# Performance work log

Measured on AMD Instinct MI355X. Metric: run time of the kernel, lower is better.

Reference implementation:

```python
import jax, jax.numpy as jnp
import numpy as np

B, T, D_IN, D_OUT = 4, 2048, 1024, 1024

def setup_inputs() -> dict:
    key = jax.random.key(0)
    k0, k1, k2, k3 = jax.random.split(key, 4)
    s = 1.0 / np.sqrt(D_IN)
    return {
        "x": jax.random.normal(k0, (B, T, D_IN), dtype=jnp.float32),
        "w_query": jax.random.normal(k1, (D_OUT, D_IN), dtype=jnp.float32) * s,
        "w_key": jax.random.normal(k2, (D_OUT, D_IN), dtype=jnp.float32) * s,
        "w_value": jax.random.normal(k3, (D_OUT, D_IN), dtype=jnp.float32) * s,
    }

def reference(x, w_query, w_key, w_value):
    # Linear (no bias): y = x @ W.T, W has shape (d_out, d_in)
    q = jnp.einsum('btd,od->bto', x, w_query)   # (B,T,d_out)
    k = jnp.einsum('btd,od->bto', x, w_key)
    v = jnp.einsum('btd,od->bto', x, w_value)
    scale = 1.0 / jnp.sqrt(jnp.asarray(k.shape[-1], dtype=x.dtype))
    scores = jnp.einsum('bqo,bko->bqk', q, k) * scale  # (B,T,T)
    t = scores.shape[-1]
    causal = jnp.tril(jnp.ones((t, t), dtype=bool))    # True = keep
    scores = jnp.where(causal, scores, -jnp.inf)
    weights = jax.nn.softmax(scores, axis=-1)
    # dropout rate is 0.0 -> identity
    context = jnp.einsum('bqk,bko->bqo', weights, v)   # (B,T,d_out)
    return context
```

## Files before the change

### kernel.cpp

```cpp
#include <hip/hip_runtime.h>
#include <hip/hip_bf16.h>

#define NB 4
#define TT 2048
#define DD 1024
#define MM (NB*TT)

using f32x4  = __attribute__((ext_vector_type(4))) float;
using bf16x8 = __attribute__((ext_vector_type(8))) __bf16;
using u16x8  = __attribute__((ext_vector_type(8))) unsigned short;

__device__ __forceinline__ unsigned short f2b(float f) {
  __hip_bfloat16 h = __float2bfloat16(f);
  return *reinterpret_cast<unsigned short*>(&h);
}

__device__ __forceinline__ float b2f(unsigned short u) {
  __hip_bfloat16 h = *reinterpret_cast<__hip_bfloat16*>(&u);
  return __bfloat162float(h);
}

__device__ __forceinline__ void gld_lds16(const void* g, void* l) {
  __builtin_amdgcn_global_load_lds(
      (const __attribute__((address_space(1))) void*)g,
      (__attribute__((address_space(3))) void*)l, 16, 0, 0);
}

__global__ void k_cvt(const float* __restrict__ src, unsigned short* __restrict__ dst, int n4) {
  int i = blockIdx.x * blockDim.x + threadIdx.x;
  int stride = gridDim.x * blockDim.x;
  for (; i < n4; i += stride) {
    float4 v = reinterpret_cast<const float4*>(src)[i];
    ushort4 o;
    o.x = f2b(v.x); o.y = f2b(v.y); o.z = f2b(v.z); o.w = f2b(v.w);
    reinterpret_cast<ushort4*>(dst)[i] = o;
  }
}

__launch_bounds__(256)
__global__ void k_qkv(const unsigned short* __restrict__ xb,
                      const unsigned short* __restrict__ wqb,
                      const unsigned short* __restrict__ wkb,
                      const unsigned short* __restrict__ wvb,
                      unsigned short* __restrict__ Qb,
                      unsigned short* __restrict__ Kb,
                      unsigned short* __restrict__ Vt) {
  __shared__ __align__(16) unsigned short As[128*32];
  __shared__ __align__(16) unsigned short Bs[128*32];
  const int tid = threadIdx.x;
  const int l = tid & 63, wid = tid >> 6;
  const int z = blockIdx.z;
  const unsigned short* W = (z == 0) ? wqb : (z == 1) ? wkb : wvb;
  unsigned short* out = (z == 0) ? Qb : (z == 1) ? Kb : Vt;
  const long m0 = (long)blockIdx.x * 128;
  const long n0 = (long)blockIdx.y * 128;
  const int l15 = l & 15, l4 = l >> 4;
  const int wr = (wid >> 1) * 64, wc = (wid & 1) * 64;

  const int lrow = tid >> 2;
  const int lcol = (tid & 3) * 8;
  const unsigned short* Ap = xb + (m0 + lrow) * DD + lcol;
  const unsigned short* Wp = W  + (n0 + lrow) * DD + lcol;
  unsigned short* AsW = &As[wid * 512];
  unsigned short* BsW = &Bs[wid * 512];

  f32x4 acc[4][4] = {};

  for (int k0 = 0; k0 < DD; k0 += 32) {
    __syncthreads();
    gld_lds16(Ap + k0,           AsW);
    gld_lds16(Ap + 64*DD + k0,   AsW + 2048);
    gld_lds16(Wp + k0,           BsW);
    gld_lds16(Wp + 64*DD + k0,   BsW + 2048);
    __syncthreads();
    bf16x8 af[4], bfr[4];
    #pragma unroll
    for (int mi = 0; mi < 4; ++mi)
      af[mi] = *reinterpret_cast<const bf16x8*>(&As[(wr + mi*16 + l15)*32 + l4*8]);
    #pragma unroll
    for (int ni = 0; ni < 4; ++ni)
      bfr[ni] = *reinterpret_cast<const bf16x8*>(&Bs[(wc + ni*16 + l15)*32 + l4*8]);
    #pragma unroll
    for (int mi = 0; mi < 4; ++mi)
      #pragma unroll
      for (int ni = 0; ni < 4; ++ni)
        acc[mi][ni] = __builtin_amdgcn_mfma_f32_16x16x32_bf16(af[mi], bfr[ni], acc[mi][ni], 0, 0, 0);
  }

  if (z < 2) {
    #pragma unroll
    for (int mi = 0; mi < 4; ++mi)
      #pragma unroll
      for (int ni = 0; ni < 4; ++ni)
        #pragma unroll
        for (int r = 0; r < 4; ++r) {
          long row = m0 + wr + mi*16 + l4*4 + r;
          long col = n0 + wc + ni*16 + l15;
          out[row * DD + col] = f2b(acc[mi][ni][r]);
        }
  } else {
    #pragma unroll
    for (int mi = 0; mi < 4; ++mi)
      #pragma unroll
      for (int ni = 0; ni < 4; ++ni)
        #pragma unroll
        for (int r = 0; r < 4; ++r) {
          long row = m0 + wr + mi*16 + l4*4 + r;
          long col = n0 + wc + ni*16 + l15;
          long b = row >> 11, t = row & (TT - 1);
          out[(b * DD + col) * TT + t] = f2b(acc[mi][ni][r]);
        }
  }
}

__launch_bounds__(256)
__global__ void k_scores(const unsigned short* __restrict__ Qb,
                         const unsigned short* __restrict__ Kb,
                         unsigned short* __restrict__ S) {
  __shared__ __align__(16) unsigned short As[128*32];
  __shared__ __align__(16) unsigned short Bs[128*32];
  const int tid = threadIdx.x;
  const int l = tid & 63, wid = tid >> 6;
  const int l15 = l & 15, l4 = l >> 4;
  const int wr = (wid >> 1) * 64, wc = (wid & 1) * 64;

  const int b = blockIdx.x / 136;
  int t = blockIdx.x % 136;
  int qi = 0;
  while ((qi + 1) * (qi + 2) / 2 <= t) qi++;
  const int ki = t - qi * (qi + 1) / 2;

  const size_t arow0 = (size_t)b * TT + qi * 128;
  const size_t brow0 = (size_t)b * TT + ki * 128;

  const int lrow = tid >> 2;
  const int lcol = (tid & 3) * 8;
  const unsigned short* Ap = Qb + (arow0 + lrow) * DD + lcol;
  const unsigned short* Bp = Kb + (brow0 + lrow) * DD + lcol;
  unsigned short* AsW = &As[wid * 512];
  unsigned short* BsW = &Bs[wid * 512];

  f32x4 acc[4][4] = {};

  for (int k0 = 0; k0 < DD; k0 += 32) {
    __syncthreads();
    gld_lds16(Ap + k0,           AsW);
    gld_lds16(Ap + 64*DD + k0,   AsW + 2048);
    gld_lds16(Bp + k0,           BsW);
    gld_lds16(Bp + 64*DD + k0,   BsW + 2048);
    __syncthreads();
    bf16x8 af[4], bfr[4];
    #pragma unroll
    for (int mi = 0; mi < 4; ++mi)
      af[mi] = *reinterpret_cast<const bf16x8*>(&As[(wr + mi*16 + l15)*32 + l4*8]);
    #pragma unroll
    for (int ni = 0; ni < 4; ++ni)
      bfr[ni] = *reinterpret_cast<const bf16x8*>(&Bs[(wc + ni*16 + l15)*32 + l4*8]);
    #pragma unroll
    for (int mi = 0; mi < 4; ++mi)
      #pragma unroll
      for (int ni = 0; ni < 4; ++ni)
        acc[mi][ni] = __builtin_amdgcn_mfma_f32_16x16x32_bf16(af[mi], bfr[ni], acc[mi][ni], 0, 0, 0);
  }

  const float scale = 0.03125f;
  #pragma unroll
  for (int mi = 0; mi < 4; ++mi)
    #pragma unroll
    for (int ni = 0; ni < 4; ++ni)
      #pragma unroll
      for (int r = 0; r < 4; ++r) {
        int row = wr + mi*16 + l4*4 + r;
        int col = wc + ni*16 + l15;
        int gq = qi*128 + row, gk = ki*128 + col;
        float v = (gk > gq) ? -1e30f : acc[mi][ni][r] * scale;
        S[((size_t)b * TT + gq) * TT + gk] = f2b(v);
      }
}

__launch_bounds__(256)
__global__ void k_softmax(unsigned short* __restrict__ S, float* __restrict__ rl) {
  const int tid = threadIdx.x;
  const int w = tid >> 6, l = tid & 63;
  const int row = blockIdx.x * 4 + w;
  const int b = row >> 11, q = row & (TT - 1);
  unsigned short* Srow = S + ((size_t)b * TT + q) * TT;
  const int width = ((q >> 7) + 1) << 7;

  float v[4][8];
  bool has[4];
  float mx = -1e30f;
  #pragma unroll
  for (int c = 0; c < 4; ++c) {
    const int off = c * 512 + l * 8;
    has[c] = off < width;
    if (has[c]) {
      u16x8 u = *reinterpret_cast<const u16x8*>(&Srow[off]);
      #pragma unroll
      for (int j = 0; j < 8; ++j) { v[c][j] = b2f(u[j]); mx = fmaxf(mx, v[c][j]); }
    }
  }
  #pragma unroll
  for (int mm = 1; mm < 64; mm <<= 1) mx = fmaxf(mx, __shfl_xor(mx, mm));

  float s = 0.f;
  #pragma unroll
  for (int c = 0; c < 4; ++c) {
    if (has[c]) {
      u16x8 u;
      #pragma unroll
      for (int j = 0; j < 8; ++j) {
        float p = __expf(v[c][j] - mx);
        s += p;
        u[j] = f2b(p);
      }
      *reinterpret_cast<u16x8*>(&Srow[c * 512 + l * 8]) = u;
    }
  }
  #pragma unroll
  for (int mm = 1; mm < 64; mm <<= 1) s += __shfl_xor(s, mm);
  if (l == 0) rl[row] = 1.0f / s;
}

__launch_bounds__(256)
__global__ void k_pv(const unsigned short* __restrict__ P,
                     const unsigned short* __restrict__ Vt,
                     const float* __restrict__ rl,
                     float* __restrict__ O) {
  __shared__ __align__(16) unsigned short As[128*32];
  __shared__ __align__(16) unsigned short Bs[128*32];
  const int tid = threadIdx.x;
  const int l = tid & 63, wid = tid >> 6;
  const int l15 = l & 15, l4 = l >> 4;
  const int wr = (wid >> 1) * 64, wc = (wid & 1) * 64;

  const int qi = 15 - (blockIdx.x >> 5);
  const int di = (blockIdx.x >> 2) & 7;
  const int b  = blockIdx.x & 3;
  const int KEXT = (qi + 1) * 128;

  const int lrow = tid >> 2;
  const int lcol = (tid & 3) * 8;
  const unsigned short* Ap = P  + ((size_t)b * TT + qi * 128 + lrow) * TT + lcol;
  const unsigned short* Bp = Vt + ((size_t)b * DD + di * 128 + lrow) * TT + lcol;
  unsigned short* AsW = &As[wid * 512];
  unsigned short* BsW = &Bs[wid * 512];

  f32x4 acc[4][4] = {};

  for (int k0 = 0; k0 < KEXT; k0 += 32) {
    __syncthreads();
    gld_lds16(Ap + k0,           AsW);
    gld_lds16(Ap + 64*TT + k0,   AsW + 2048);
    gld_lds16(Bp + k0,           BsW);
    gld_lds16(Bp + 64*TT + k0,   BsW + 2048);
    __syncthreads();
    bf16x8 af[4], bfr[4];
    #pragma unroll
    for (int mi = 0; mi < 4; ++mi)
      af[mi] = *reinterpret_cast<const bf16x8*>(&As[(wr + mi*16 + l15)*32 + l4*8]);
    #pragma unroll
    for (int ni = 0; ni < 4; ++ni)
      bfr[ni] = *reinterpret_cast<const bf16x8*>(&Bs[(wc + ni*16 + l15)*32 + l4*8]);
    #pragma unroll
    for (int mi = 0; mi < 4; ++mi)
      #pragma unroll
      for (int ni = 0; ni < 4; ++ni)
        acc[mi][ni] = __builtin_amdgcn_mfma_f32_16x16x32_bf16(af[mi], bfr[ni], acc[mi][ni], 0, 0, 0);
  }

  #pragma unroll
  for (int mi = 0; mi < 4; ++mi)
    #pragma unroll
    for (int ni = 0; ni < 4; ++ni)
      #pragma unroll
      for (int r = 0; r < 4; ++r) {
        int row = wr + mi*16 + l4*4 + r;
        int col = wc + ni*16 + l15;
        size_t q = (size_t)qi * 128 + row;
        O[((size_t)b * TT + q) * DD + di * 128 + col] =
            acc[mi][ni][r] * rl[(size_t)b * TT + q];
      }
}

extern "C" void kernel_launch(void* const* d_in, const int* in_sizes, int n_in,
                              void* d_out, int out_size, void* d_ws, size_t ws_size,
                              hipStream_t stream) {
  const float* x  = (const float*)d_in[0];
  const float* wq = (const float*)d_in[1];
  const float* wk = (const float*)d_in[2];
  const float* wv = (const float*)d_in[3];
  unsigned short* ws  = (unsigned short*)d_ws;
  unsigned short* Qb  = ws;
  unsigned short* Kb  = Qb + (size_t)MM * DD;
  unsigned short* Vt  = Kb + (size_t)MM * DD;
  unsigned short* Sb  = Vt + (size_t)MM * DD;
  unsigned short* xb  = Sb;
  unsigned short* wqb = xb + (size_t)MM * DD;
  unsigned short* wkb = wqb + (size_t)DD * DD;
  unsigned short* wvb = wkb + (size_t)DD * DD;
  float* rl = (float*)(Sb + (size_t)NB * TT * TT);
  float* out = (float*)d_out;

  k_cvt<<<1024, 256, 0, stream>>>(x,  xb,  MM*DD/4);
  k_cvt<<<256,  256, 0, stream>>>(wq, wqb, DD*DD/4);
  k_cvt<<<256,  256, 0, stream>>>(wk, wkb, DD*DD/4);
  k_cvt<<<256,  256, 0, stream>>>(wv, wvb, DD*DD/4);
  k_qkv<<<dim3(MM/128, DD/128, 3), 256, 0, stream>>>(xb, wqb, wkb, wvb, Qb, Kb, Vt);
  k_scores<<<544, 256, 0, stream>>>(Qb, Kb, Sb);
  k_softmax<<<MM/4, 256, 0, stream>>>(Sb, rl);
  k_pv<<<512, 256, 0, stream>>>(Sb, Vt, rl, out);
}
```

Before: 187.4 us.

## Rewrite QKV projection as 256x256 double-buffered GEMM and fuse conversion kernels

Merges the four fp32-to-bf16 conversion launches into one kernel. Replaces the 128x128 single-buffered QKV GEMM with a 256x256 tile, 8-wave kernel that uses 128KB of LDS. Global-to-LDS loads are double-buffered with a K tile of 64, and prefetch is interleaved with split MFMA phases through raw barriers, waitcnt and setprio. LDS reads use an XOR swizzle to avoid bank conflicts. The aim is to hide memory latency and raise MFMA utilization, at the cost of complex manual synchronization and a smaller grid of 384 blocks, about one wave on 256 CUs.

```diff
diff --git a/kernel.cpp b/kernel.cpp
--- a/kernel.cpp
+++ b/kernel.cpp
@@ -26,89 +26,187 @@
       (__attribute__((address_space(3))) void*)l, 16, 0, 0);
 }
 
-__global__ void k_cvt(const float* __restrict__ src, unsigned short* __restrict__ dst, int n4) {
+__device__ __forceinline__ void bar() {
+  asm volatile("" ::: "memory");
+  __builtin_amdgcn_s_barrier();
+  asm volatile("" ::: "memory");
+}
+
+__global__ void k_cvt4(const float* __restrict__ x,  const float* __restrict__ wq,
+                       const float* __restrict__ wk, const float* __restrict__ wv,
+                       unsigned short* __restrict__ xb, unsigned short* __restrict__ wqb,
+                       unsigned short* __restrict__ wkb, unsigned short* __restrict__ wvb) {
+  const int nx = MM*DD/4, nw = DD*DD/4;
+  const int ntot = nx + 3*nw;
   int i = blockIdx.x * blockDim.x + threadIdx.x;
   int stride = gridDim.x * blockDim.x;
-  for (; i < n4; i += stride) {
-    float4 v = reinterpret_cast<const float4*>(src)[i];
+  for (; i < ntot; i += stride) {
+    const float* s; unsigned short* d; int j;
+    if (i < nx)            { s = x;  d = xb;  j = i; }
+    else if (i < nx + nw)  { s = wq; d = wqb; j = i - nx; }
+    else if (i < nx + 2*nw){ s = wk; d = wkb; j = i - nx - nw; }
+    else                   { s = wv; d = wvb; j = i - nx - 2*nw; }
+    float4 v = reinterpret_cast<const float4*>(s)[j];
     ushort4 o;
     o.x = f2b(v.x); o.y = f2b(v.y); o.z = f2b(v.z); o.w = f2b(v.w);
-    reinterpret_cast<ushort4*>(dst)[i] = o;
-  }
-}
-
-__launch_bounds__(256)
-__global__ void k_qkv(const unsigned short* __restrict__ xb,
-                      const unsigned short* __restrict__ wqb,
-                      const unsigned short* __restrict__ wkb,
-                      const unsigned short* __restrict__ wvb,
-                      unsigned short* __restrict__ Qb,
-                      unsigned short* __restrict__ Kb,
-                      unsigned short* __restrict__ Vt) {
-  __shared__ __align__(16) unsigned short As[128*32];
-  __shared__ __align__(16) unsigned short Bs[128*32];
+    reinterpret_cast<ushort4*>(d)[j] = o;
+  }
+}
+
+__launch_bounds__(512, 2)
+__global__ void k_qkv8(const unsigned short* __restrict__ xb,
+                       const unsigned short* __restrict__ wqb,
+                       const unsigned short* __restrict__ wkb,
+                       const unsigned short* __restrict__ wvb,
+                       unsigned short* __restrict__ Qb,
+                       unsigned short* __restrict__ Kb,
+                       unsigned short* __restrict__ Vt) {
+  __shared__ __align__(16) char Lds[131072];
   const int tid = threadIdx.x;
   const int l = tid & 63, wid = tid >> 6;
+  const int l15 = l & 15, l4 = l >> 4;
+  const int wm = wid >> 2, wn = wid & 3;
   const int z = blockIdx.z;
   const unsigned short* W = (z == 0) ? wqb : (z == 1) ? wkb : wvb;
-  unsigned short* out = (z == 0) ? Qb : (z == 1) ? Kb : Vt;
-  const long m0 = (long)blockIdx.x * 128;
-  const long n0 = (long)blockIdx.y * 128;
-  const int l15 = l & 15, l4 = l >> 4;
-  const int wr = (wid >> 1) * 64, wc = (wid & 1) * 64;
-
-  const int lrow = tid >> 2;
-  const int lcol = (tid & 3) * 8;
-  const unsigned short* Ap = xb + (m0 + lrow) * DD + lcol;
-  const unsigned short* Wp = W  + (n0 + lrow) * DD + lcol;
-  unsigned short* AsW = &As[wid * 512];
-  unsigned short* BsW = &Bs[wid * 512];
-
-  f32x4 acc[4][4] = {};
-
-  for (int k0 = 0; k0 < DD; k0 += 32) {
-    __syncthreads();
-    gld_lds16(Ap + k0,           AsW);
-    gld_lds16(Ap + 64*DD + k0,   AsW + 2048);
-    gld_lds16(Wp + k0,           BsW);
-    gld_lds16(Wp + 64*DD + k0,   BsW + 2048);
-    __syncthreads();
-    bf16x8 af[4], bfr[4];
-    #pragma unroll
-    for (int mi = 0; mi < 4; ++mi)
-      af[mi] = *reinterpret_cast<const bf16x8*>(&As[(wr + mi*16 + l15)*32 + l4*8]);
-    #pragma unroll
-    for (int ni = 0; ni < 4; ++ni)
-      bfr[ni] = *reinterpret_cast<const bf16x8*>(&Bs[(wc + ni*16 + l15)*32 + l4*8]);
-    #pragma unroll
-    for (int mi = 0; mi < 4; ++mi)
-      #pragma unroll
-      for (int ni = 0; ni < 4; ++ni)
-        acc[mi][ni] = __builtin_amdgcn_mfma_f32_16x16x32_bf16(af[mi], bfr[ni], acc[mi][ni], 0, 0, 0);
-  }
+  const size_t m0 = (size_t)blockIdx.x * 256;
+  const size_t n0 = (size_t)blockIdx.y * 256;
+
+  int srow[2], scb[2];
+  #pragma unroll
+  for (int j = 0; j < 2; ++j) {
+    int d  = (j*512 + tid) * 16;
+    int sd = d ^ (((d >> 9) & 1) << 5);
+    srow[j] = sd >> 7;
+    scb[j]  = sd & 127;
+  }
+  const char* pA[2][2]; const char* pB[2][2];
+  #pragma unroll
+  for (int h = 0; h < 2; ++h)
+    #pragma unroll
+    for (int j = 0; j < 2; ++j) {
+      pA[h][j] = (const char*)xb + ((m0 + h*128 + srow[j]) * DD) * 2 + scb[j];
+      pB[h][j] = (const char*)W  + ((n0 + h*128 + srow[j]) * DD) * 2 + scb[j];
+    }
+  char* ldsA = Lds;
+  char* ldsB = Lds + 65536;
+
+#define STG(p, ldsr, slot, half, kt) do {                                         \
+    gld_lds16(p[half][0] + (size_t)(kt)*128,                                      \
+              (ldsr) + (slot)*32768 + (half)*16384 + wid*1024);                   \
+    gld_lds16(p[half][1] + (size_t)(kt)*128,                                      \
+              (ldsr) + (slot)*32768 + (half)*16384 + 8192 + wid*1024);            \
+  } while (0)
+
+#define KTQ 16
+  STG(pA, ldsA, 0, 0, 0);
+  STG(pA, ldsA, 0, 1, 0);
+  STG(pB, ldsB, 0, 0, 0);
+  STG(pB, ldsB, 0, 1, 0);
+  STG(pA, ldsA, 1, 0, 1);
+  STG(pA, ldsA, 1, 1, 1);
+  STG(pB, ldsB, 1, 0, 1);
+  asm volatile("s_waitcnt vmcnt(6)" ::: "memory");
+  bar();
+
+  f32x4 acc[8][4] = {};
+  bf16x8 af[8][2], bf[2][2];
+
+#define TILE(t, S) do {                                                           \
+    const int tn = ((t)+1 < KTQ) ? (t)+1 : 0;                                     \
+    const int t2 = ((t)+2 < KTQ) ? (t)+2 : 0;                                     \
+           \
+    _Pragma("unroll") for (int m = 0; m < 8; ++m)                                 \
+      _Pragma("unroll") for (int kk = 0; kk < 2; ++kk) {                          \
+        int lg = m*2048 + l15*128 + kk*64 + l4*16;                                \
+        int ph = lg ^ (((lg >> 9) & 1) << 5);                                     \
+        af[m][kk] = *(const bf16x8*)(ldsA + (S)*32768 + wm*16384 + ph); }         \
+    _Pragma("unroll") for (int n = 0; n < 2; ++n)                                 \
+      _Pragma("unroll") for (int kk = 0; kk < 2; ++kk) {                          \
+        int lg = ((wn&1)*64 + n*16 + l15)*128 + kk*64 + l4*16;                    \
+        int ph = lg ^ (((lg >> 9) & 1) << 5);                                     \
+        bf[n][kk] = *(const bf16x8*)(ldsB + (S)*32768 + (wn>>1)*16384 + ph); }    \
+    STG(pB, ldsB, (S)^1, 1, tn);                                                  \
+    bar();                                                                        \
+    asm volatile("s_waitcnt lgkmcnt(0)" ::: "memory");                            \
+    __builtin_amdgcn_sched_barrier(0);                                            \
+    __builtin_amdgcn_s_setprio(1);                                                \
+    _Pragma("unroll") for (int m = 0; m < 4; ++m)                                 \
+      _Pragma("unroll") for (int n = 0; n < 2; ++n)                               \
+        _Pragma("unroll") for (int kk = 0; kk < 2; ++kk)                          \
+          acc[m][n] = __builtin_amdgcn_mfma_f32_16x16x32_bf16(af[m][kk], bf[n][kk], acc[m][n], 0,0,0); \
+    __builtin_amdgcn_s_setprio(0);                                                \
+    bar();                                                                        \
+                                           \
+    STG(pA, ldsA, S, 0, t2);                                                      \
+    bar();                                                                        \
+    __builtin_amdgcn_s_setprio(1);                                                \
+    _Pragma("unroll") for (int m = 4; m < 8; ++m)                                 \
+      _Pragma("unroll") for (int n = 0; n < 2; ++n)                               \
+        _Pragma("unroll") for (int kk = 0; kk < 2; ++kk)                          \
+          acc[m][n] = __builtin_amdgcn_mfma_f32_16x16x32_bf16(af[m][kk], bf[n][kk], acc[m][n], 0,0,0); \
+    __builtin_amdgcn_s_setprio(0);                                                \
+    bar();                                                                        \
+                            \
+    _Pragma("unroll") for (int n = 0; n < 2; ++n)                                 \
+      _Pragma("unroll") for (int kk = 0; kk < 2; ++kk) {                          \
+        int lg = ((wn&1)*64 + (n+2)*16 + l15)*128 + kk*64 + l4*16;                \
+        int ph = lg ^ (((lg >> 9) & 1) << 5);                                     \
+        bf[n][kk] = *(const bf16x8*)(ldsB + (S)*32768 + (wn>>1)*16384 + ph); }    \
+    STG(pA, ldsA, S, 1, t2);                                                      \
+    bar();                                                                        \
+    asm volatile("s_waitcnt lgkmcnt(0)" ::: "memory");                            \
+    __builtin_amdgcn_sched_barrier(0);                                            \
+    __builtin_amdgcn_s_setprio(1);                                                \
+    _Pragma("unroll") for (int m = 0; m < 4; ++m)                                 \
+      _Pragma("unroll") for (int n = 0; n < 2; ++n)                               \
+        _Pragma("unroll") for (int kk = 0; kk < 2; ++kk)                          \
+          acc[m][n+2] = __builtin_amdgcn_mfma_f32_16x16x32_bf16(af[m][kk], bf[n][kk], acc[m][n+2], 0,0,0); \
+    __builtin_amdgcn_s_setprio(0);                                                \
+    bar();                                                                        \
+                            \
+    STG(pB, ldsB, S, 0, t2);                                                      \
+    asm volatile("s_waitcnt vmcnt(6)" ::: "memory");                              \
+    bar();                                                                        \
+    __builtin_amdgcn_s_setprio(1);                                                \
+    _Pragma("unroll") for (int m = 4; m < 8; ++m)                                 \
+      _Pragma("unroll") for (int n = 0; n < 2; ++n)                               \
+        _Pragma("unroll") for (int kk = 0; kk < 2; ++kk)                          \
+          acc[m][n+2] = __builtin_amdgcn_mfma_f32_16x16x32_bf16(af[m][kk], bf[n][kk], acc[m][n+2], 0,0,0); \
+    __builtin_amdgcn_s_setprio(0);                                                \
+    bar();                                                                        \
+  } while (0)
+
+  for (int tp = 0; tp < KTQ; tp += 2) {
+    TILE(tp, 0);
+    TILE(tp + 1, 1);
+  }
+#undef TILE
+#undef STG
+  asm volatile("s_waitcnt vmcnt(0)" ::: "memory");
 
   if (z < 2) {
-    #pragma unroll
-    for (int mi = 0; mi < 4; ++mi)
-      #pragma unroll
-      for (int ni = 0; ni < 4; ++ni)
+    unsigned short* out = (z == 0) ? Qb : Kb;
+    #pragma unroll
+    for (int m = 0; m < 8; ++m)
+      #pragma unroll
+      for (int n = 0; n < 4; ++n)
         #pragma unroll
         for (int r = 0; r < 4; ++r) {
-          long row = m0 + wr + mi*16 + l4*4 + r;
-          long col = n0 + wc + ni*16 + l15;
-          out[row * DD + col] = f2b(acc[mi][ni][r]);
+          size_t row = m0 + wm*128 + m*16 + l4*4 + r;
+          size_t col = n0 + wn*64  + n*16 + l15;
+          out[row * DD + col] = f2b(acc[m][n][r]);
         }
   } else {
     #pragma unroll
-    for (int mi = 0; mi < 4; ++mi)
-      #pragma unroll
-      for (int ni = 0; ni < 4; ++ni)
+    for (int m = 0; m < 8; ++m)
+      #pragma unroll
+      for (int n = 0; n < 4; ++n)
         #pragma unroll
         for (int r = 0; r < 4; ++r) {
-          long row = m0 + wr + mi*16 + l4*4 + r;
-          long col = n0 + wc + ni*16 + l15;
-          long b = row >> 11, t = row & (TT - 1);
-          out[(b * DD + col) * TT + t] = f2b(acc[mi][ni][r]);
+          size_t row = m0 + wm*128 + m*16 + l4*4 + r;
+          size_t col = n0 + wn*64  + n*16 + l15;
+          size_t b = row >> 11, t = row & (TT - 1);
+          Vt[(b * DD + col) * TT + t] = f2b(acc[m][n][r]);
         }
   }
 }
@@ -302,11 +400,8 @@
   float* rl = (float*)(Sb + (size_t)NB * TT * TT);
   float* out = (float*)d_out;
 
-  k_cvt<<<1024, 256, 0, stream>>>(x,  xb,  MM*DD/4);
-  k_cvt<<<256,  256, 0, stream>>>(wq, wqb, DD*DD/4);
-  k_cvt<<<256,  256, 0, stream>>>(wk, wkb, DD*DD/4);
-  k_cvt<<<256,  256, 0, stream>>>(wv, wvb, DD*DD/4);
-  k_qkv<<<dim3(MM/128, DD/128, 3), 256, 0, stream>>>(xb, wqb, wkb, wvb, Qb, Kb, Vt);
+  k_cvt4<<<2048, 256, 0, stream>>>(x, wq, wk, wv, xb, wqb, wkb, wvb);
+  k_qkv8<<<dim3(32, 4, 3), 512, 0, stream>>>(xb, wqb, wkb, wvb, Qb, Kb, Vt);
   k_scores<<<544, 256, 0, stream>>>(Qb, Kb, Sb);
   k_softmax<<<MM/4, 256, 0, stream>>>(Sb, rl);
   k_pv<<<512, 256, 0, stream>>>(Sb, Vt, rl, out);
```

Result: slower. 197.5 us (+5.4%).
